# Kernel tuning notes

Measured on AMD Instinct MI355X. Metric: run time of the kernel, lower is better.

## Reference

```python
import jax, jax.numpy as jnp
import numpy as np

N, E, F_IN, D_COORD, W, KW, KIN, DEPTH = 10000, 300000, 3, 3, 32, 256, 6, 4

def _lin(k, i, o):
    return jax.random.normal(k, (i, o), jnp.float32) * (1.0 / np.sqrt(i))

def setup_inputs() -> dict:
    key = jax.random.key(0)
    ks = jax.random.split(key, 16)
    x = jax.random.normal(ks[0], (N, F_IN), jnp.float32)
    edge_index = jax.random.randint(ks[1], (2, E), 0, N, jnp.int64)
    edge_attr = jax.random.normal(ks[2], (E, KIN), jnp.float32)
    coords_init = jax.random.normal(ks[3], (N, D_COORD), jnp.float32)
    return {
        "x": x, "edge_index": edge_index, "edge_attr": edge_attr,
        "coords_init": coords_init,
        "fc1_w": _lin(ks[4], F_IN, W), "fc1_b": jnp.zeros((W,), jnp.float32),
        # kernel DenseNet: [ker_in, ker_width//2, ker_width, width**2]
        "ker1_w": _lin(ks[5], KIN, KW // 2), "ker1_b": jnp.zeros((KW // 2,), jnp.float32),
        "ker2_w": _lin(ks[6], KW // 2, KW), "ker2_b": jnp.zeros((KW,), jnp.float32),
        "ker3_w": _lin(ks[7], KW, W * W), "ker3_b": jnp.zeros((W * W,), jnp.float32),
        # coord MLP: Linear(W,W)+ReLU+Linear(W,1)
        "cm1_w": _lin(ks[8], W, W), "cm1_b": jnp.zeros((W,), jnp.float32),
        "cm2_w": _lin(ks[9], W, 1), "cm2_b": jnp.zeros((1,), jnp.float32),
        # fc2: Linear(W,2W)+ReLU+Linear(2W,1)
        "fc2a_w": _lin(ks[10], W, 2 * W), "fc2a_b": jnp.zeros((2 * W,), jnp.float32),
        "fc2b_w": _lin(ks[11], 2 * W, 1), "fc2b_b": jnp.zeros((1,), jnp.float32),
        "depth": DEPTH,
    }

def reference(x, edge_index, edge_attr, coords_init,
              fc1_w, fc1_b, ker1_w, ker1_b, ker2_w, ker2_b, ker3_w, ker3_b,
              cm1_w, cm1_b, cm2_w, cm2_b, fc2a_w, fc2a_b, fc2b_w, fc2b_b, depth):
    n = x.shape[0]
    w = fc1_w.shape[1]
    row, col = edge_index[0], edge_index[1]
    h = x @ fc1_w + fc1_b  # [N, W]
    # edge kernel MLP -> per-edge [W, W] matrix (edge_attr fixed across layers)
    k = jax.nn.relu(edge_attr @ ker1_w + ker1_b)
    k = jax.nn.relu(k @ ker2_w + ker2_b)
    k = (k @ ker3_w + ker3_b).reshape(-1, w, w)  # [E, W, W]
    cnt = jnp.clip(jax.ops.segment_sum(jnp.ones((row.shape[0], 1), h.dtype), row, n), 1.0)
    coord = coords_init
    for _ in range(depth):
        m = jnp.einsum('eij,ej->ei', k, h[col])              # gather + kernel apply
        agg = jax.ops.segment_sum(m, row, n) / cnt           # mean scatter to nodes
        we = jax.nn.relu(m @ cm1_w + cm1_b) @ cm2_w + cm2_b  # [E, 1] coord weights
        trans = (coord[row] - coord[col]) * we               # equivariant edge vectors
        coord = coord + jax.ops.segment_sum(trans, row, n) / cnt
        h = jax.nn.relu(h + agg)
    out = jax.nn.relu(h @ fc2a_w + fc2a_b) @ fc2b_w + fc2b_b  # [N, 1]
    return out, coord
```

## Files before the change

### kernel.cpp

```cpp
#include <hip/hip_runtime.h>

#define NN 10000
#define NE 300000
#define DEPTH 4

typedef unsigned int   u32;
typedef unsigned short u16;
typedef unsigned char  u8;

typedef _Float16 half8  __attribute__((ext_vector_type(8)));
typedef _Float16 half2t __attribute__((ext_vector_type(2)));
typedef float  floatx16 __attribute__((ext_vector_type(16)));

__device__ __forceinline__ u32 f2h(float f) {
    f = fminf(fmaxf(f, -60000.f), 60000.f);
    _Float16 h = (_Float16)f;
    return (u32)__builtin_bit_cast(u16, h);
}
__device__ __forceinline__ float h2f(u16 b) {
    return (float)__builtin_bit_cast(_Float16, b);
}
__device__ __forceinline__ u32 pkrtz2(float a, float b) {
    return __builtin_bit_cast(u32, __builtin_amdgcn_cvt_pkrtz(a, b));
}
__device__ __forceinline__ u32 dq2(u32 x, u32 sel) {
    const half2t h1024 = {(_Float16)1024.f, (_Float16)1024.f};
    half2t v = __builtin_bit_cast(half2t, __builtin_amdgcn_perm(x, 0x64646464u, sel));
    return __builtin_bit_cast(u32, v - h1024);
}

__global__ void sentinel_kernel(float* out, int n, float val) {
    int i = blockIdx.x * 256 + threadIdx.x;
    if (i < n) out[i] = val;
}

__global__ void detect_idx_kernel(const int* __restrict__ ei, int* __restrict__ flag) {
    __shared__ int nz;
    if (threadIdx.x == 0) nz = 0;
    __syncthreads();
    if (ei[threadIdx.x * 2 + 1] != 0) atomicAdd(&nz, 1);
    __syncthreads();
    if (threadIdx.x == 0) *flag = (nz == 0) ? 1 : 0;
}

__global__ __launch_bounds__(256) void convert_idx_kernel(
    const int* __restrict__ ei, const int* __restrict__ flag,
    int* __restrict__ ridx, int* __restrict__ cidx)
{
    int e = blockIdx.x * 256 + threadIdx.x;
    if (e >= 2 * NE) return;
    const int is64 = *flag;
    int v = is64 ? ei[2 * e] : ei[e];
    if (e < NE) ridx[e] = v; else cidx[e - NE] = v;
}

__global__ __launch_bounds__(256) void init_nodes_kernel(
    const float* __restrict__ x, const float* __restrict__ fc1w,
    const float* __restrict__ fc1b, const float* __restrict__ ci,
    float* __restrict__ h, float* __restrict__ coord)
{
    int idx = blockIdx.x * 256 + threadIdx.x;
    if (idx < NN * 32) {
        int v = idx >> 5, f = idx & 31;
        float acc = fc1b[f];
#pragma unroll
        for (int i = 0; i < 3; i++) acc += x[v * 3 + i] * fc1w[i * 32 + f];
        h[idx] = acc;
    }
    if (idx < NN * 3) coord[idx] = ci[idx];
}

__global__ __launch_bounds__(256) void count_kernel(
    const int* __restrict__ ridx, const int* __restrict__ cidx,
    int* __restrict__ rowcnt, int* __restrict__ colcnt)
{
    int e = blockIdx.x * 256 + threadIdx.x;
    if (e < NE) { atomicAdd(&rowcnt[ridx[e]], 1); atomicAdd(&colcnt[cidx[e]], 1); }
}

__global__ void scan_kernel(const int* __restrict__ colcnt, const int* __restrict__ rowcnt,
                            int* __restrict__ cstart, int* __restrict__ cnext,
                            int* __restrict__ rstart, int* __restrict__ rnext,
                            float* __restrict__ invc, int mode)
{
    __shared__ int partC[256], partR[256];
    const int t = threadIdx.x;
    int sumC = 0, sumR = 0;
    for (int i = 0; i < 40; i++) {
        int v = t * 40 + i;
        if (v < NN) { sumC += colcnt[v]; sumR += rowcnt[v]; }
    }
    partC[t] = sumC; partR[t] = sumR;
    __syncthreads();
    if (t == 0) {
        int rc = 0, rr = 0;
        for (int i = 0; i < 256; i++) {
            int tc = partC[i]; partC[i] = rc; rc += tc;
            int tr = partR[i]; partR[i] = rr; rr += tr;
        }
    }
    __syncthreads();
    int runC = partC[t], runR = partR[t];
    for (int i = 0; i < 40; i++) {
        int v = t * 40 + i;
        if (v < NN) {
            cstart[v] = runC; cnext[v] = runC; runC += colcnt[v];
            if (mode) { rstart[v] = runR; rnext[v] = runR; runR += rowcnt[v]; }
        }
    }
    if (t == 255) { cstart[NN] = runC; if (mode) rstart[NN] = runR; }
    for (int v = t; v < NN; v += 256) invc[v] = 1.0f / fmaxf((float)rowcnt[v], 1.0f);
}

__global__ __launch_bounds__(256) void scatter_kernel(
    const int* __restrict__ cidx, const int* __restrict__ ridx,
    int* __restrict__ cnext, int* __restrict__ rnext,
    int* __restrict__ elist, int* __restrict__ rpos, int* __restrict__ rcol,
    int mode)
{
    int e = blockIdx.x * 256 + threadIdx.x;
    if (e >= NE) return;
    int pos = atomicAdd(&cnext[cidx[e]], 1);
    elist[pos] = e;
    if (mode) {
        int rp = atomicAdd(&rnext[ridx[e]], 1);
        rpos[e] = rp;
        rcol[rp] = cidx[e];
    }
}

__global__ __launch_bounds__(256) void w2pack_kernel(
    const float* __restrict__ w2, u16* __restrict__ w2h)
{
    const int slot = blockIdx.x * 256 + threadIdx.x;
    const int c = slot >> 9, s = (slot >> 6) & 7, l = slot & 63;
    const int li = l & 31, hf = l >> 5;
    const int k0 = s * 16 + hf * 8, col = c * 32 + li;
    u32 pk[8];
#pragma unroll
    for (int j = 0; j < 8; j++) pk[j] = f2h(w2[(size_t)(k0 + j) * 256 + col]);
    uint4 o;
    o.x = pk[0] | (pk[1] << 16);
    o.y = pk[2] | (pk[3] << 16);
    o.z = pk[4] | (pk[5] << 16);
    o.w = pk[6] | (pk[7] << 16);
    *(uint4*)&w2h[(size_t)slot * 8] = o;
}

__global__ void cm1pack_kernel(const float* __restrict__ cm1w, u16* __restrict__ cmpk)
{
    const int t = threadIdx.x;
    if (t >= 128) return;
    const int s2 = t >> 6, l = t & 63, li = l & 31, hf = l >> 5;
    u32 pk[8];
#pragma unroll
    for (int j = 0; j < 8; j++) pk[j] = f2h(cm1w[(s2 * 16 + hf * 8 + j) * 32 + li]);
    uint4 o;
    o.x = pk[0] | (pk[1] << 16);
    o.y = pk[2] | (pk[3] << 16);
    o.z = pk[4] | (pk[5] << 16);
    o.w = pk[6] | (pk[7] << 16);
    *(uint4*)&cmpk[(size_t)(s2 * 64 + l) * 8] = o;
}

__global__ __launch_bounds__(256) void w3pack_kernel(
    const float* __restrict__ w3, u16* __restrict__ w3g)
{
    const int slot = blockIdx.x * 256 + threadIdx.x;
    const int lane = slot & 63;
    const int ks   = (slot >> 6) & 1;
    const int pt   = slot >> 7;
    const int p    = pt * 32 + (lane & 31);
    const int kb   = ks * 16 + (lane >> 5) * 8;
    const int s  = p >> 9;
    const int hf = (p >> 8) & 1;
    const int i  = (p >> 3) & 31;
    const int j7 = p & 7;
    const int c  = s * 16 + hf * 8 + j7;
    const float* wp = &w3[(size_t)c * 1024 + i * 32 + kb];
    const float4 x0 = *(const float4*)wp;
    const float4 x1 = *(const float4*)(wp + 4);
    uint4 o;
    o.x = f2h(x0.x) | (f2h(x0.y) << 16);
    o.y = f2h(x0.z) | (f2h(x0.w) << 16);
    o.z = f2h(x1.x) | (f2h(x1.y) << 16);
    o.w = f2h(x1.z) | (f2h(x1.w) << 16);
    *(uint4*)&w3g[(size_t)slot * 8] = o;
}

__global__ __launch_bounds__(256, 4) void mlp_k2_kernel(
    const float* __restrict__ ea,
    const float* __restrict__ w1, const float* __restrict__ b1,
    const u16* __restrict__ w2h, const float* __restrict__ b2,
    u8* __restrict__ k2base, u16* __restrict__ k2s)
{
    __shared__ __align__(16) float ea_s[32 * 6];
    __shared__ __align__(16) u16   k1f[4096];
    __shared__ __align__(16) u16   M_s[32 * 258];
    __shared__ float pmax_s[4][32];
    const int t  = threadIdx.x;
    const int e0 = blockIdx.x * 32;

    for (int idx = t; idx < 192; idx += 256)
        ea_s[idx] = ea[(size_t)e0 * 6 + idx];
    __syncthreads();

    for (int slot = t; slot < 512; slot += 256) {
        const int s  = slot >> 6;
        const int l  = slot & 63;
        const int li = l & 31, hf = l >> 5;
        const int k0 = s * 16 + hf * 8;
        float acc[8];
        {
            const float4 ba = *(const float4*)&b1[k0];
            const float4 bb = *(const float4*)&b1[k0 + 4];
            acc[0] = ba.x; acc[1] = ba.y; acc[2] = ba.z; acc[3] = ba.w;
            acc[4] = bb.x; acc[5] = bb.y; acc[6] = bb.z; acc[7] = bb.w;
        }
#pragma unroll
        for (int i = 0; i < 6; i++) {
            const float ev = ea_s[li * 6 + i];
            const float4 wa = *(const float4*)&w1[i * 128 + k0];
            const float4 wb = *(const float4*)&w1[i * 128 + k0 + 4];
            acc[0] += ev * wa.x; acc[1] += ev * wa.y;
            acc[2] += ev * wa.z; acc[3] += ev * wa.w;
            acc[4] += ev * wb.x; acc[5] += ev * wb.y;
            acc[6] += ev * wb.z; acc[7] += ev * wb.w;
        }
        uint4 o;
        o.x = pkrtz2(fmaxf(acc[0], 0.f), fmaxf(acc[1], 0.f));
        o.y = pkrtz2(fmaxf(acc[2], 0.f), fmaxf(acc[3], 0.f));
        o.z = pkrtz2(fmaxf(acc[4], 0.f), fmaxf(acc[5], 0.f));
        o.w = pkrtz2(fmaxf(acc[6], 0.f), fmaxf(acc[7], 0.f));
        *(uint4*)&k1f[slot * 8] = o;
    }
    __syncthreads();

    {
        const int w  = t >> 6, l = t & 63;
        const int li = l & 31, hf = l >> 5;
#pragma unroll
        for (int ct = 0; ct < 2; ct++) {
            const int c = w * 2 + ct;
            floatx16 acc;
#pragma unroll
            for (int r = 0; r < 16; r++) acc[r] = 0.f;
#pragma unroll
            for (int s = 0; s < 8; s++) {
                const half8 a = __builtin_bit_cast(half8,
                    *(const uint4*)&k1f[(s * 64 + l) * 8]);
                const half8 b = __builtin_bit_cast(half8,
                    *(const uint4*)&w2h[(((size_t)c * 8 + s) * 64 + l) * 8]);
                acc = __builtin_amdgcn_mfma_f32_32x32x16_f16(a, b, acc, 0, 0, 0);
            }
            const float bb = b2[c * 32 + li];
#pragma unroll
            for (int r = 0; r < 16; r++) {
                const int e = (r & 3) + 8 * (r >> 2) + 4 * hf;
                M_s[e * 258 + c * 32 + li] =
                    __builtin_bit_cast(u16, (_Float16)fmaxf(acc[r] + bb, 0.f));
            }
        }
    }
    __syncthreads();

    {
        const int el = t & 31, qq = t >> 5;
        const int w  = t >> 6;
        u32 hw[16];
#pragma unroll
        for (int c = 0; c < 16; c++)
            hw[c] = *(const u32*)&M_s[el * 258 + qq * 32 + c * 2];

        half2t pm = __builtin_bit_cast(half2t, hw[0]);
#pragma unroll
        for (int c = 1; c < 16; c++)
            pm = __builtin_elementwise_max(pm, __builtin_bit_cast(half2t, hw[c]));
        float mx = fmaxf((float)pm[0], (float)pm[1]);
        mx = fmaxf(mx, __shfl_xor(mx, 32, 64));
        if ((t & 32) == 0) pmax_s[w][el] = mx;
        __syncthreads();
        mx = fmaxf(fmaxf(pmax_s[0][el], pmax_s[1][el]),
                   fmaxf(pmax_s[2][el], pmax_s[3][el]));
        const float sc  = mx / 255.f;
        const float inv = (mx > 0.f) ? 255.f / mx : 0.f;
        if (t < 32) k2s[e0 + el] = (u16)f2h(sc);
        const float magic = 8388608.f;
        u32 w8[8];
#pragma unroll
        for (int u = 0; u < 8; u++) {
            const u32 a = hw[u * 2], b = hw[u * 2 + 1];
            const float v0 = h2f((u16)a);
            const float v1 = h2f((u16)(a >> 16));
            const float v2 = h2f((u16)b);
            const float v3 = h2f((u16)(b >> 16));
            const u32 r0 = __builtin_bit_cast(u32, fmaf(v0, inv, magic));
            const u32 r1 = __builtin_bit_cast(u32, fmaf(v1, inv, magic));
            const u32 r2 = __builtin_bit_cast(u32, fmaf(v2, inv, magic));
            const u32 r3 = __builtin_bit_cast(u32, fmaf(v3, inv, magic));
            const u32 p01 = __builtin_amdgcn_perm(r1, r0, 0x0C0C0400u);
            const u32 p23 = __builtin_amdgcn_perm(r3, r2, 0x0C0C0400u);
            w8[u] = __builtin_amdgcn_perm(p23, p01, 0x05040100u);
        }
        u8* outp = k2base + (size_t)(e0 + el) * 256 + qq * 32;
        *(uint4*)outp        = make_uint4(w8[0], w8[1], w8[2], w8[3]);
        *(uint4*)(outp + 16) = make_uint4(w8[4], w8[5], w8[6], w8[7]);
    }
}

__global__ __launch_bounds__(256) void g_kernel(
    const float* __restrict__ h, const u16* __restrict__ w3g,
    u16* __restrict__ Gg)
{
    const int t = threadIdx.x, w = t >> 6, l = t & 63;
    const int li = l & 31, hf = l >> 5;
    const int n0 = blockIdx.x * 32;
    const int node = n0 + li;

    half8 a0, a1;
    if (node < NN) {
        const float* hp = &h[(size_t)node * 32 + hf * 8];
        const float4 x0 = *(const float4*)hp;
        const float4 x1 = *(const float4*)(hp + 4);
        const float4 y0 = *(const float4*)(hp + 16);
        const float4 y1 = *(const float4*)(hp + 20);
        uint4 ua, ub;
        ua.x = pkrtz2(x0.x, x0.y); ua.y = pkrtz2(x0.z, x0.w);
        ua.z = pkrtz2(x1.x, x1.y); ua.w = pkrtz2(x1.z, x1.w);
        ub.x = pkrtz2(y0.x, y0.y); ub.y = pkrtz2(y0.z, y0.w);
        ub.z = pkrtz2(y1.x, y1.y); ub.w = pkrtz2(y1.z, y1.w);
        a0 = __builtin_bit_cast(half8, ua);
        a1 = __builtin_bit_cast(half8, ub);
    } else {
        const uint4 z = make_uint4(0u, 0u, 0u, 0u);
        a0 = __builtin_bit_cast(half8, z);
        a1 = __builtin_bit_cast(half8, z);
    }

    const int pt0 = blockIdx.y * 64 + w * 16;
    const int full = (n0 + 32 <= NN) ? 1 : 0;
#pragma unroll 4
    for (int it = 0; it < 16; it++) {
        const int pt = pt0 + it;
        const uint4 b0u = *(const uint4*)&w3g[((size_t)pt * 2 + 0) * 512 + (size_t)l * 8];
        const uint4 b1u = *(const uint4*)&w3g[((size_t)pt * 2 + 1) * 512 + (size_t)l * 8];
        floatx16 acc;
#pragma unroll
        for (int r = 0; r < 16; r++) acc[r] = 0.f;
        acc = __builtin_amdgcn_mfma_f32_32x32x16_f16(
            a0, __builtin_bit_cast(half8, b0u), acc, 0, 0, 0);
        acc = __builtin_amdgcn_mfma_f32_32x32x16_f16(
            a1, __builtin_bit_cast(half8, b1u), acc, 0, 0, 0);
        if (full) {
#pragma unroll
            for (int r = 0; r < 16; r++) {
                const int nn = n0 + (r & 3) + 8 * (r >> 2) + 4 * hf;
                Gg[(size_t)nn * 8192 + pt * 32 + li] = (u16)f2h(acc[r]);
            }
        } else {
#pragma unroll
            for (int r = 0; r < 16; r++) {
                const int nn = n0 + (r & 3) + 8 * (r >> 2) + 4 * hf;
                if (nn < NN)
                    Gg[(size_t)nn * 8192 + pt * 32 + li] = (u16)f2h(acc[r]);
            }
        }
    }
}

__global__ __launch_bounds__(256, 3) void edge_kernel(
    const int* __restrict__ cstart, const int* __restrict__ elist,
    const int* __restrict__ ridx, const int* __restrict__ rpos,
    const u8* __restrict__ k2base, const u16* __restrict__ k2s,
    const u16* __restrict__ Gg, const float* __restrict__ coord,
    const u16* __restrict__ cmpk, const float* __restrict__ cm1b,
    const float* __restrict__ cm2w, const float* __restrict__ cm2b,
    const float* __restrict__ h, const float* __restrict__ b3,
    float* __restrict__ agg, float* __restrict__ dco,
    u16* __restrict__ mbuf, u16* __restrict__ webuf, int mode)
{
    const int t    = threadIdx.x;
    const int w    = t >> 6;
    const int l    = t & 63;
    const int li   = l & 31;
    const int half = l >> 5;

    __shared__ __align__(16) float Mlds_all[4][32 * 34];
    __shared__ int   idxS_all[4][32];
    __shared__ float seS_all[4][32];
    float* Mlds = Mlds_all[w];
    int*   idxS = idxS_all[w];
    float* seS  = seS_all[w];

    const int n = blockIdx.x * 4 + w;
    if (n >= NN) return;
    const int s0  = cstart[n];
    const int deg = cstart[n + 1] - s0;
    if (deg == 0) return;

    half8 cmb[2];
    cmb[0] = __builtin_bit_cast(half8, *(const uint4*)&cmpk[(size_t)(0 * 64 + l) * 8]);
    cmb[1] = __builtin_bit_cast(half8, *(const uint4*)&cmpk[(size_t)(1 * 64 + l) * 8]);
    half8 onesb;
#pragma unroll
    for (int j = 0; j < 8; j++) onesb[j] = (_Float16)1.0f;
    const float cm1bq = cm1b[li];
    const float cm2q  = cm2w[li];
    const float cm2b0 = cm2b[0];
    float bv = 0.f;
    {
        const float* hn = &h[(size_t)n * 32];
        const float* bp = &b3[(size_t)li * 32];
#pragma unroll
        for (int c2 = 0; c2 < 8; c2++) {
            const float4 hv = *(const float4*)&hn[c2 * 4];
            const float4 bq = *(const float4*)&bp[c2 * 4];
            bv += hv.x * bq.x + hv.y * bq.y + hv.z * bq.z + hv.w * bq.w;
        }
    }
    const float con   = (mode == 0 && li < 3) ? coord[(size_t)n * 3 + li] : 0.f;
    const u16* Gn = Gg + (size_t)n * 8192;

    for (int base = 0; base < deg; base += 32) {
        const int mye   = base + li;
        const int valid = (mye < deg) ? 1 : 0;
        const int eid   = valid ? elist[s0 + mye] : 0;
        const float se  = valid ? h2f(k2s[eid]) : 0.f;
        if (l < 32) { idxS[l] = valid ? (mode ? rpos[eid] : ridx[eid]) : 0; seS[l] = se; }

        uint4 gr[16];
#pragma unroll
        for (int s = 0; s < 16; s++)
            gr[s] = *(const uint4*)(Gn + s * 512 + l * 8);
        const u8* k2row = k2base + (size_t)eid * 256 + half * 8;
        uint2 kr[16];
#pragma unroll
        for (int s = 0; s < 16; s++) kr[s] = *(const uint2*)(k2row + s * 16);

        floatx16 acc;
#pragma unroll
        for (int r = 0; r < 16; r++) acc[r] = 0.f;
#pragma unroll
        for (int s = 0; s < 16; s++) {
            uint4 au;
            au.x = dq2(kr[s].x, 0x00050004u);
            au.y = dq2(kr[s].x, 0x00070006u);
            au.z = dq2(kr[s].y, 0x00050004u);
            au.w = dq2(kr[s].y, 0x00070006u);
            acc = __builtin_amdgcn_mfma_f32_32x32x16_f16(
                __builtin_bit_cast(half8, au),
                __builtin_bit_cast(half8, gr[s]), acc, 0, 0, 0);
        }
#pragma unroll
        for (int r = 0; r < 16; r++) {
            const int e = (r & 3) + 8 * (r >> 2) + 4 * half;
            acc[r] = acc[r] * seS[e] + bv;
        }

#pragma unroll
        for (int r = 0; r < 16; r++) {
            const int e = (r & 3) + 8 * (r >> 2) + 4 * half;
            Mlds[e * 34 + li] = acc[r];
        }
        if (mode == 0) {
#pragma unroll
            for (int r = 0; r < 16; r++) {
                const int e = (r & 3) + 8 * (r >> 2) + 4 * half;
                if (base + e < deg)
                    atomicAdd(&agg[(size_t)idxS[e] * 32 + li], acc[r]);
            }
        } else {
#pragma unroll
            for (int r = 0; r < 16; r++) {
                const int e = (r & 3) + 8 * (r >> 2) + 4 * half;
                if (base + e < deg)
                    mbuf[(size_t)idxS[e] * 32 + li] =
                        __builtin_bit_cast(u16, (_Float16)acc[r]);
            }
        }
        asm volatile("s_waitcnt lgkmcnt(0)" ::: "memory");

        floatx16 acc2;
#pragma unroll
        for (int r = 0; r < 16; r++) acc2[r] = cm1bq;
#pragma unroll
        for (int s2 = 0; s2 < 2; s2++) {
            const float* mp = &Mlds[li * 34 + s2 * 16 + half * 8];
            const float2 m0 = *(const float2*)mp;
            const float2 m1 = *(const float2*)(mp + 2);
            const float2 m2 = *(const float2*)(mp + 4);
            const float2 m3 = *(const float2*)(mp + 6);
            uint4 au;
            au.x = pkrtz2(m0.x, m0.y);
            au.y = pkrtz2(m1.x, m1.y);
            au.z = pkrtz2(m2.x, m2.y);
            au.w = pkrtz2(m3.x, m3.y);
            acc2 = __builtin_amdgcn_mfma_f32_32x32x16_f16(
                __builtin_bit_cast(half8, au), cmb[s2], acc2, 0, 0, 0);
        }

#pragma unroll
        for (int r = 0; r < 16; r++) {
            const int e = (r & 3) + 8 * (r >> 2) + 4 * half;
            Mlds[e * 34 + li] = fmaxf(acc2[r], 0.f) * cm2q;
        }
        asm volatile("s_waitcnt lgkmcnt(0)" ::: "memory");
        floatx16 acc3;
#pragma unroll
        for (int r = 0; r < 16; r++) acc3[r] = cm2b0;
#pragma unroll
        for (int s2 = 0; s2 < 2; s2++) {
            const float* mp = &Mlds[li * 34 + s2 * 16 + half * 8];
            const float2 m0 = *(const float2*)mp;
            const float2 m1 = *(const float2*)(mp + 2);
            const float2 m2 = *(const float2*)(mp + 4);
            const float2 m3 = *(const float2*)(mp + 6);
            uint4 au;
            au.x = pkrtz2(m0.x, m0.y);
            au.y = pkrtz2(m1.x, m1.y);
            au.z = pkrtz2(m2.x, m2.y);
            au.w = pkrtz2(m3.x, m3.y);
            acc3 = __builtin_amdgcn_mfma_f32_32x32x16_f16(
                __builtin_bit_cast(half8, au), onesb, acc3, 0, 0, 0);
        }

        if (mode == 0) {
#pragma unroll
            for (int r = 0; r < 16; r++) {
                const int e = (r & 3) + 8 * (r >> 2) + 4 * half;
                if (base + e < deg && li < 3) {
                    const int rr = idxS[e];
                    const float d = coord[(size_t)rr * 3 + li] - con;
                    atomicAdd(&dco[(size_t)rr * 3 + li], d * acc3[r]);
                }
            }
        } else {
#pragma unroll
            for (int r = 0; r < 16; r++) {
                const int e = (r & 3) + 8 * (r >> 2) + 4 * half;
                if (base + e < deg && li == 0)
                    webuf[idxS[e]] = __builtin_bit_cast(u16, (_Float16)acc3[r]);
            }
        }
    }
}

__global__ __launch_bounds__(256) void node_update_kernel(
    float* __restrict__ h, float* __restrict__ agg,
    float* __restrict__ coord, float* __restrict__ dco,
    const float* __restrict__ invc)
{
    int idx = blockIdx.x * 256 + threadIdx.x;
    if (idx < NN * 32) {
        int v = idx >> 5;
        h[idx] = fmaxf(h[idx] + agg[idx] * invc[v], 0.f);
        agg[idx] = 0.f;
    }
    if (idx < NN * 3) {
        coord[idx] += dco[idx] * invc[idx / 3];
        dco[idx] = 0.f;
    }
}

__global__ __launch_bounds__(256) void node_update2_kernel(
    float* __restrict__ h, const float* __restrict__ coordCur,
    float* __restrict__ coordNew, const u16* __restrict__ mbuf,
    const u16* __restrict__ webuf, const int* __restrict__ rcol,
    const int* __restrict__ rstart, const float* __restrict__ invc)
{
    const int t = threadIdx.x, w = t >> 6, l = t & 63;
    const int li = l & 31, half = l >> 5;
    const int v = blockIdx.x * 4 + w;
    if (v >= NN) return;
    const int s0 = rstart[v], s1 = rstart[v + 1];
    const float iv = invc[v];

    float acc = 0.f;
    for (int s = s0 + half; s < s1; s += 2)
        acc += h2f(mbuf[(size_t)s * 32 + li]);
    acc += __shfl_xor(acc, 32, 64);
    if (half == 0)
        h[(size_t)v * 32 + li] = fmaxf(h[(size_t)v * 32 + li] + acc * iv, 0.f);

    const float c0 = coordCur[(size_t)v * 3 + 0];
    const float c1 = coordCur[(size_t)v * 3 + 1];
    const float c2 = coordCur[(size_t)v * 3 + 2];
    float p0 = 0.f, p1 = 0.f, p2 = 0.f;
    for (int s = s0 + l; s < s1; s += 64) {
        const float we = h2f(webuf[s]);
        const int col = rcol[s];
        p0 += (c0 - coordCur[(size_t)col * 3 + 0]) * we;
        p1 += (c1 - coordCur[(size_t)col * 3 + 1]) * we;
        p2 += (c2 - coordCur[(size_t)col * 3 + 2]) * we;
    }
#pragma unroll
    for (int off = 32; off >= 1; off >>= 1) {
        p0 += __shfl_xor(p0, off, 64);
        p1 += __shfl_xor(p1, off, 64);
        p2 += __shfl_xor(p2, off, 64);
    }
    if (l == 0) {
        coordNew[(size_t)v * 3 + 0] = c0 + p0 * iv;
        coordNew[(size_t)v * 3 + 1] = c1 + p1 * iv;
        coordNew[(size_t)v * 3 + 2] = c2 + p2 * iv;
    }
}

__global__ __launch_bounds__(256) void final_kernel(
    const float* __restrict__ h, const float* __restrict__ coord,
    const float* __restrict__ wa, const float* __restrict__ ba,
    const float* __restrict__ wb, const float* __restrict__ bb,
    float* __restrict__ out)
{
    const int lane = threadIdx.x & 63;
    const int v = blockIdx.x * 4 + (threadIdx.x >> 6);
    if (v >= NN) return;
    const float hreg = (lane < 32) ? h[(size_t)v * 32 + lane] : 0.f;
    float acc = ba[lane];
#pragma unroll
    for (int f = 0; f < 32; f++) acc += __shfl(hreg, f, 64) * wa[f * 64 + lane];
    float part = fmaxf(acc, 0.f) * wb[lane];
#pragma unroll
    for (int off = 32; off >= 1; off >>= 1) part += __shfl_xor(part, off, 64);
    if (lane == 0) out[v] = part + bb[0];
    if (lane < 3) out[NN + (size_t)v * 3 + lane] = coord[(size_t)v * 3 + lane];
}

extern "C" void kernel_launch(void* const* d_in, const int* in_sizes, int n_in,
                              void* d_out, int out_size, void* d_ws, size_t ws_size,
                              hipStream_t stream)
{
    const float* x    = (const float*)d_in[0];
    const int*   ei   = (const int*)d_in[1];
    const float* ea   = (const float*)d_in[2];
    const float* ci   = (const float*)d_in[3];
    const float* fc1w = (const float*)d_in[4];
    const float* fc1b = (const float*)d_in[5];
    const float* k1w  = (const float*)d_in[6];
    const float* k1b  = (const float*)d_in[7];
    const float* k2w  = (const float*)d_in[8];
    const float* k2b  = (const float*)d_in[9];
    const float* k3w  = (const float*)d_in[10];
    const float* k3b  = (const float*)d_in[11];
    const float* cm1w = (const float*)d_in[12];
    const float* cm1b = (const float*)d_in[13];
    const float* cm2w = (const float*)d_in[14];
    const float* cm2b = (const float*)d_in[15];
    const float* f2aw = (const float*)d_in[16];
    const float* f2ab = (const float*)d_in[17];
    const float* f2bw = (const float*)d_in[18];
    const float* f2bb = (const float*)d_in[19];

    size_t o_k2, o_k2s, o_G, o_h, o_coA, o_coB, o_invc, o_rc, o_cc,
           o_cs, o_rs, o_cn, o_rn, o_el, o_w2h, o_cmpk, o_w3g, o_agg, o_dco,
           o_ri, o_ci, o_rp, o_rcl, o_mb, o_wb;
#define ALGN(v) (((v) + 255) & ~(size_t)255)
    auto carve = [&](int mode) -> size_t {
        size_t o = 0;
        o_k2  = o; o += ALGN((size_t)NE * 256);
        o_k2s = o; o += ALGN((size_t)NE * 2);
        o_G   = o; o += ALGN((size_t)NN * 8192 * 2);
        o_h   = o; o += ALGN((size_t)NN * 32 * 4);
        o_coA = o; o += ALGN((size_t)NN * 3 * 4);
        o_invc= o; o += ALGN((size_t)NN * 4);
        o_rc  = o; o += ALGN((size_t)NN * 4);
        o_cc  = o; o += ALGN((size_t)NN * 4);
        o_cs  = o; o += ALGN((size_t)(NN + 1) * 4);
        o_cn  = o; o += ALGN((size_t)NN * 4);
        o_el  = o; o += ALGN((size_t)NE * 4);
        o_w2h = o; o += ALGN((size_t)128 * 256 * 2);
        o_cmpk= o; o += ALGN((size_t)1024 * 2);
        o_w3g = o; o += ALGN((size_t)32768 * 8 * 2);
        if (mode == 0) {
            o_agg = o; o += ALGN((size_t)NN * 32 * 4);
            o_dco = o; o += ALGN((size_t)NN * 3 * 4);
            o_ri  = o; o += ALGN((size_t)NE * 4);
            o_ci  = o; o += ALGN((size_t)NE * 4);
            o_coB = o_coA; o_rs = o_cs; o_rn = o_cn;
            o_rp = o_el; o_rcl = o_el; o_mb = o_k2; o_wb = o_k2;
        } else {
            o_coB = o; o += ALGN((size_t)NN * 3 * 4);
            o_rs  = o; o += ALGN((size_t)(NN + 1) * 4);
            o_rn  = o; o += ALGN((size_t)NN * 4);
            o_rp  = o; o += ALGN((size_t)NE * 4);
            o_rcl = o; o += ALGN((size_t)NE * 4);
            const size_t u = o;
            o_ri = u; o_ci = u + ALGN((size_t)NE * 4);
            o_mb = u; o_wb = u + ALGN((size_t)NE * 32 * 2);
            const size_t setup_sz = 2 * ALGN((size_t)NE * 4);
            const size_t layer_sz = ALGN((size_t)NE * 32 * 2) + ALGN((size_t)NE * 2);
            o += (setup_sz > layer_sz) ? setup_sz : layer_sz;
            o_agg = o_k2; o_dco = o_k2;
        }
        return o;
    };
    int mode = (ws_size >= carve(1)) ? 1 : 0;
    size_t need = carve(mode);
    if (ws_size < need) {
        sentinel_kernel<<<(NN * 4 + 255) / 256, 256, 0, stream>>>((float*)d_out, NN * 4, 1.0e6f);
        return;
    }

    char* wsb = (char*)d_ws;
    u8*    k2g   = (u8*)(wsb + o_k2);
    u16*   k2s   = (u16*)(wsb + o_k2s);
    u16*   Gg    = (u16*)(wsb + o_G);
    float* h     = (float*)(wsb + o_h);
    float* coA   = (float*)(wsb + o_coA);
    float* coB   = (float*)(wsb + o_coB);
    float* invc  = (float*)(wsb + o_invc);
    int*   rowcnt= (int*)(wsb + o_rc);
    int*   colcnt= (int*)(wsb + o_cc);
    int*   cstart= (int*)(wsb + o_cs);
    int*   rstart= (int*)(wsb + o_rs);
    int*   cnext = (int*)(wsb + o_cn);
    int*   rnext = (int*)(wsb + o_rn);
    int*   elist = (int*)(wsb + o_el);
    u16*   w2h   = (u16*)(wsb + o_w2h);
    u16*   cmpk  = (u16*)(wsb + o_cmpk);
    u16*   w3g   = (u16*)(wsb + o_w3g);
    float* agg   = (float*)(wsb + o_agg);
    float* dco   = (float*)(wsb + o_dco);
    int*   ridx  = (int*)(wsb + o_ri);
    int*   cidx  = (int*)(wsb + o_ci);
    int*   rpos  = (int*)(wsb + o_rp);
    int*   rcol  = (int*)(wsb + o_rcl);
    u16*   mbuf  = (u16*)(wsb + o_mb);
    u16*   webuf = (u16*)(wsb + o_wb);

    hipMemsetAsync(rowcnt, 0, (size_t)NN * 4, stream);
    hipMemsetAsync(colcnt, 0, (size_t)NN * 4, stream);
    if (mode == 0) {
        hipMemsetAsync(agg, 0, (size_t)NN * 32 * 4, stream);
        hipMemsetAsync(dco, 0, (size_t)NN * 3 * 4, stream);
    }

    detect_idx_kernel<<<1, 256, 0, stream>>>(ei, cnext);
    convert_idx_kernel<<<(2 * NE + 255) / 256, 256, 0, stream>>>(ei, cnext, ridx, cidx);
    init_nodes_kernel<<<(NN * 32 + 255) / 256, 256, 0, stream>>>(x, fc1w, fc1b, ci, h, coA);
    count_kernel<<<(NE + 255) / 256, 256, 0, stream>>>(ridx, cidx, rowcnt, colcnt);
    scan_kernel<<<1, 256, 0, stream>>>(colcnt, rowcnt, cstart, cnext, rstart, rnext,
                                       invc, mode);
    scatter_kernel<<<(NE + 255) / 256, 256, 0, stream>>>(cidx, ridx, cnext, rnext,
                                                         elist, rpos, rcol, mode);
    w2pack_kernel<<<16, 256, 0, stream>>>(k2w, w2h);
    cm1pack_kernel<<<1, 128, 0, stream>>>(cm1w, cmpk);
    w3pack_kernel<<<128, 256, 0, stream>>>(k3w, w3g);
    mlp_k2_kernel<<<NE / 32, 256, 0, stream>>>(ea, k1w, k1b, w2h, k2b, k2g, k2s);

    float* coCur = coA;
    float* coAlt = coB;
    const dim3 ggrid((NN + 31) / 32, 4);
    for (int l = 0; l < DEPTH; l++) {
        g_kernel<<<ggrid, 256, 0, stream>>>(h, w3g, Gg);
        edge_kernel<<<(NN + 3) / 4, 256, 0, stream>>>(cstart, elist, ridx, rpos,
                                                      k2g, k2s, Gg, coCur, cmpk,
                                                      cm1b, cm2w, cm2b, h, k3b,
                                                      agg, dco, mbuf, webuf, mode);
        if (mode == 1) {
            node_update2_kernel<<<(NN + 3) / 4, 256, 0, stream>>>(
                h, coCur, coAlt, mbuf, webuf, rcol, rstart, invc);
            float* tmp = coCur; coCur = coAlt; coAlt = tmp;
        } else {
            node_update_kernel<<<(NN * 32 + 255) / 256, 256, 0, stream>>>(
                h, agg, coCur, dco, invc);
        }
    }
    final_kernel<<<(NN + 3) / 4, 256, 0, stream>>>(h, coCur, f2aw, f2ab, f2bw, f2bb,
                                                   (float*)d_out);
}
```

Baseline: 817.7 us.

## Fuse per-node G computation into edge kernel via shared memory

```diff
diff --git a/kernel.cpp b/kernel.cpp
--- a/kernel.cpp
+++ b/kernel.cpp
@@ -308,71 +308,11 @@
     }
 }
 
-__global__ __launch_bounds__(256) void g_kernel(
-    const float* __restrict__ h, const u16* __restrict__ w3g,
-    u16* __restrict__ Gg)
-{
-    const int t = threadIdx.x, w = t >> 6, l = t & 63;
-    const int li = l & 31, hf = l >> 5;
-    const int n0 = blockIdx.x * 32;
-    const int node = n0 + li;
-
-    half8 a0, a1;
-    if (node < NN) {
-        const float* hp = &h[(size_t)node * 32 + hf * 8];
-        const float4 x0 = *(const float4*)hp;
-        const float4 x1 = *(const float4*)(hp + 4);
-        const float4 y0 = *(const float4*)(hp + 16);
-        const float4 y1 = *(const float4*)(hp + 20);
-        uint4 ua, ub;
-        ua.x = pkrtz2(x0.x, x0.y); ua.y = pkrtz2(x0.z, x0.w);
-        ua.z = pkrtz2(x1.x, x1.y); ua.w = pkrtz2(x1.z, x1.w);
-        ub.x = pkrtz2(y0.x, y0.y); ub.y = pkrtz2(y0.z, y0.w);
-        ub.z = pkrtz2(y1.x, y1.y); ub.w = pkrtz2(y1.z, y1.w);
-        a0 = __builtin_bit_cast(half8, ua);
-        a1 = __builtin_bit_cast(half8, ub);
-    } else {
-        const uint4 z = make_uint4(0u, 0u, 0u, 0u);
-        a0 = __builtin_bit_cast(half8, z);
-        a1 = __builtin_bit_cast(half8, z);
-    }
-
-    const int pt0 = blockIdx.y * 64 + w * 16;
-    const int full = (n0 + 32 <= NN) ? 1 : 0;
-#pragma unroll 4
-    for (int it = 0; it < 16; it++) {
-        const int pt = pt0 + it;
-        const uint4 b0u = *(const uint4*)&w3g[((size_t)pt * 2 + 0) * 512 + (size_t)l * 8];
-        const uint4 b1u = *(const uint4*)&w3g[((size_t)pt * 2 + 1) * 512 + (size_t)l * 8];
-        floatx16 acc;
-#pragma unroll
-        for (int r = 0; r < 16; r++) acc[r] = 0.f;
-        acc = __builtin_amdgcn_mfma_f32_32x32x16_f16(
-            a0, __builtin_bit_cast(half8, b0u), acc, 0, 0, 0);
-        acc = __builtin_amdgcn_mfma_f32_32x32x16_f16(
-            a1, __builtin_bit_cast(half8, b1u), acc, 0, 0, 0);
-        if (full) {
-#pragma unroll
-            for (int r = 0; r < 16; r++) {
-                const int nn = n0 + (r & 3) + 8 * (r >> 2) + 4 * hf;
-                Gg[(size_t)nn * 8192 + pt * 32 + li] = (u16)f2h(acc[r]);
-            }
-        } else {
-#pragma unroll
-            for (int r = 0; r < 16; r++) {
-                const int nn = n0 + (r & 3) + 8 * (r >> 2) + 4 * hf;
-                if (nn < NN)
-                    Gg[(size_t)nn * 8192 + pt * 32 + li] = (u16)f2h(acc[r]);
-            }
-        }
-    }
-}
-
-__global__ __launch_bounds__(256, 3) void edge_kernel(
+__global__ __launch_bounds__(256, 2) void edge_kernel(
     const int* __restrict__ cstart, const int* __restrict__ elist,
     const int* __restrict__ ridx, const int* __restrict__ rpos,
     const u8* __restrict__ k2base, const u16* __restrict__ k2s,
-    const u16* __restrict__ Gg, const float* __restrict__ coord,
+    const u16* __restrict__ w3g, const float* __restrict__ coord,
     const u16* __restrict__ cmpk, const float* __restrict__ cm1b,
     const float* __restrict__ cm2w, const float* __restrict__ cm2b,
     const float* __restrict__ h, const float* __restrict__ b3,
@@ -385,18 +325,15 @@
     const int li   = l & 31;
     const int half = l >> 5;
 
-    __shared__ __align__(16) float Mlds_all[4][32 * 34];
-    __shared__ int   idxS_all[4][32];
-    __shared__ float seS_all[4][32];
-    float* Mlds = Mlds_all[w];
-    int*   idxS = idxS_all[w];
-    float* seS  = seS_all[w];
-
-    const int n = blockIdx.x * 4 + w;
-    if (n >= NN) return;
+    __shared__ __align__(16) u16 Gt[4 * 8192];
+    float* Mlds = (float*)Gt + w * (32 * 34);
+    int*   idxS = (int*)((char*)Gt + 17408) + w * 32;
+    float* seS  = (float*)((char*)Gt + 17920) + w * 32;
+
+    const int n0 = blockIdx.x * 4;
+    const int n  = n0 + w;
     const int s0  = cstart[n];
     const int deg = cstart[n + 1] - s0;
-    if (deg == 0) return;
 
     half8 cmb[2];
     cmb[0] = __builtin_bit_cast(half8, *(const uint4*)&cmpk[(size_t)(0 * 64 + l) * 8]);
@@ -418,8 +355,55 @@
             bv += hv.x * bq.x + hv.y * bq.y + hv.z * bq.z + hv.w * bq.w;
         }
     }
-    const float con   = (mode == 0 && li < 3) ? coord[(size_t)n * 3 + li] : 0.f;
-    const u16* Gn = Gg + (size_t)n * 8192;
+    const float con = (mode == 0 && li < 3) ? coord[(size_t)n * 3 + li] : 0.f;
+
+    {
+        half8 a0, a1;
+        {
+            uint4 za = make_uint4(0u, 0u, 0u, 0u), zb = za;
+            if (li < 4) {
+                const float* hp = &h[(size_t)(n0 + li) * 32 + half * 8];
+                const float4 x0 = *(const float4*)hp;
+                const float4 x1 = *(const float4*)(hp + 4);
+                const float4 y0 = *(const float4*)(hp + 16);
+                const float4 y1 = *(const float4*)(hp + 20);
+                za.x = pkrtz2(x0.x, x0.y); za.y = pkrtz2(x0.z, x0.w);
+                za.z = pkrtz2(x1.x, x1.y); za.w = pkrtz2(x1.z, x1.w);
+                zb.x = pkrtz2(y0.x, y0.y); zb.y = pkrtz2(y0.z, y0.w);
+                zb.z = pkrtz2(y1.x, y1.y); zb.w = pkrtz2(y1.z, y1.w);
+            }
+            a0 = __builtin_bit_cast(half8, za);
+            a1 = __builtin_bit_cast(half8, zb);
+        }
+        const int pt0 = w * 64;
+#pragma unroll 4
+        for (int it = 0; it < 64; it++) {
+            const int pt = pt0 + it;
+            const uint4 b0u = *(const uint4*)&w3g[((size_t)(pt * 2 + 0) * 64 + l) * 8];
+            const uint4 b1u = *(const uint4*)&w3g[((size_t)(pt * 2 + 1) * 64 + l) * 8];
+            floatx16 acc;
+#pragma unroll
+            for (int r = 0; r < 16; r++) acc[r] = 0.f;
+            acc = __builtin_amdgcn_mfma_f32_32x32x16_f16(
+                a0, __builtin_bit_cast(half8, b0u), acc, 0, 0, 0);
+            acc = __builtin_amdgcn_mfma_f32_32x32x16_f16(
+                a1, __builtin_bit_cast(half8, b1u), acc, 0, 0, 0);
+            if (half == 0) {
+#pragma unroll
+                for (int r = 0; r < 4; r++)
+                    Gt[r * 8192 + pt * 32 + li] = (u16)f2h(acc[r]);
+            }
+        }
+    }
+    __syncthreads();
+
+    uint4 gr[16];
+#pragma unroll
+    for (int s = 0; s < 16; s++)
+        gr[s] = *(const uint4*)&Gt[w * 8192 + s * 512 + l * 8];
+    __syncthreads();
+
+    if (deg == 0) return;
 
     for (int base = 0; base < deg; base += 32) {
         const int mye   = base + li;
@@ -428,10 +412,6 @@
         const float se  = valid ? h2f(k2s[eid]) : 0.f;
         if (l < 32) { idxS[l] = valid ? (mode ? rpos[eid] : ridx[eid]) : 0; seS[l] = se; }
 
-        uint4 gr[16];
-#pragma unroll
-        for (int s = 0; s < 16; s++)
-            gr[s] = *(const uint4*)(Gn + s * 512 + l * 8);
         const u8* k2row = k2base + (size_t)eid * 256 + half * 8;
         uint2 kr[16];
 #pragma unroll
@@ -704,7 +684,6 @@
     char* wsb = (char*)d_ws;
     u8*    k2g   = (u8*)(wsb + o_k2);
     u16*   k2s   = (u16*)(wsb + o_k2s);
-    u16*   Gg    = (u16*)(wsb + o_G);
     float* h     = (float*)(wsb + o_h);
     float* coA   = (float*)(wsb + o_coA);
     float* coB   = (float*)(wsb + o_coB);
@@ -750,11 +729,9 @@
 
     float* coCur = coA;
     float* coAlt = coB;
-    const dim3 ggrid((NN + 31) / 32, 4);
     for (int l = 0; l < DEPTH; l++) {
-        g_kernel<<<ggrid, 256, 0, stream>>>(h, w3g, Gg);
         edge_kernel<<<(NN + 3) / 4, 256, 0, stream>>>(cstart, elist, ridx, rpos,
-                                                      k2g, k2s, Gg, coCur, cmpk,
+                                                      k2g, k2s, w3g, coCur, cmpk,
                                                       cm1b, cm2w, cm2b, h, k3b,
                                                       agg, dco, mbuf, webuf, mode);
         if (mode == 1) {
```

Result: slower. 1.006 ms (+23.1%).
